# Kernel optimization log

Hardware: AMD Instinct MI355X
Metric: run time of the kernel (lower is better)

Reference implementation:

```python
import jax, jax.numpy as jnp
import numpy as np

B, N, C, H = 32, 577, 768, 12
D = C // H  # head_dim = 64


def _rotate_half(t):
    half = t.shape[-1] // 2
    return jnp.concatenate([-t[..., half:], t[..., :half]], axis=-1)


def _rope(t, sin, cos):
    # t: [B, H, N-1, D]; sin/cos: [N-1, D] broadcast over batch and heads
    return t * cos + _rotate_half(t) * sin


def setup_inputs() -> dict:
    key = jax.random.key(0)
    ks = jax.random.split(key, 5)
    x = jax.random.normal(ks[0], (B, N, C), dtype=jnp.float32)
    w_qkv = jax.random.normal(ks[1], (C, 3 * C), dtype=jnp.float32) * (1.0 / np.sqrt(C))
    b_qkv = jnp.zeros((3 * C,), dtype=jnp.float32)
    w_proj = jax.random.normal(ks[2], (C, C), dtype=jnp.float32) * (1.0 / np.sqrt(C))
    b_proj = jnp.zeros((C,), dtype=jnp.float32)
    # rotary tables for the N-1 non-CLS tokens
    pos = jnp.arange(N - 1, dtype=jnp.float32)[:, None]            # [N-1, 1]
    inv_freq = 1.0 / (10000.0 ** (jnp.arange(0, D, 2, dtype=jnp.float32) / D))  # [D/2]
    ang = pos * inv_freq[None, :]                                   # [N-1, D/2]
    ang = jnp.concatenate([ang, ang], axis=-1)                      # [N-1, D]
    rope_sin = jnp.sin(ang)
    rope_cos = jnp.cos(ang)
    return {"x": x, "w_qkv": w_qkv, "b_qkv": b_qkv, "w_proj": w_proj,
            "b_proj": b_proj, "rope_sin": rope_sin, "rope_cos": rope_cos}


def reference(x, w_qkv, b_qkv, w_proj, b_proj, rope_sin, rope_cos):
    Bx, Nx, Cx = x.shape
    qkv = x @ w_qkv + b_qkv                                   # [B, N, 3C]
    qkv = qkv.reshape(Bx, Nx, 3, H, D).transpose(2, 0, 3, 1, 4)  # [3, B, H, N, D]
    q, k, v = qkv[0], qkv[1], qkv[2]
    # RoPE only on non-CLS tokens (index 0 is CLS)
    q = jnp.concatenate([q[:, :, :1, :], _rope(q[:, :, 1:, :], rope_sin, rope_cos)], axis=2)
    k = jnp.concatenate([k[:, :, :1, :], _rope(k[:, :, 1:, :], rope_sin, rope_cos)], axis=2)
    q = q / jnp.sqrt(jnp.float32(D))
    attn = jnp.einsum("bhqd,bhkd->bhqk", q, k)               # [B, H, N, N]
    attn = jax.nn.softmax(attn.astype(jnp.float32), axis=-1).astype(x.dtype)
    out = jnp.einsum("bhqk,bhkd->bhqd", attn, v)             # [B, H, N, D]
    out = out.transpose(0, 2, 1, 3).reshape(Bx, Nx, Cx)       # [B, N, C]
    return out @ w_proj + b_proj
```

## Files before the change

kernel.cpp:

```cpp
#include <hip/hip_runtime.h>

#define Bdim 32
#define Ndim 577
#define Cdim 768
#define Hdim 12
#define Ddim 64
#define Mdim (Bdim*Ndim)
#define VSTRIDE 640

typedef __attribute__((ext_vector_type(4))) float f32x4;
typedef __attribute__((ext_vector_type(8))) __bf16 bf16x8;
typedef __attribute__((ext_vector_type(4))) __bf16 bf16x4;

__device__ __forceinline__ void gl_lds16(const __bf16* g, __bf16* l) {
  __builtin_amdgcn_global_load_lds((const __attribute__((address_space(1))) void*)g,
                                   (__attribute__((address_space(3))) void*)l, 16, 0, 0);
}

__global__ __launch_bounds__(256) void f32_to_bf16(const float4* __restrict__ in,
                                                   bf16x4* __restrict__ out, int n4) {
  int i = blockIdx.x * 256 + threadIdx.x;
  if (i < n4) {
    float4 v = in[i];
    bf16x4 o = {(__bf16)v.x, (__bf16)v.y, (__bf16)v.z, (__bf16)v.w};
    out[i] = o;
  }
}

__global__ __launch_bounds__(256) void transpose_f32_bf16(const float* __restrict__ in,
                                                          __bf16* __restrict__ out,
                                                          int R, int Cc) {
  __shared__ float tile[64][65];
  int bx = blockIdx.x * 64;
  int by = blockIdx.y * 64;
  int tx = threadIdx.x & 63, ty = threadIdx.x >> 6;
  for (int i = ty; i < 64; i += 4) {
    int r = by + i, c = bx + tx;
    tile[i][tx] = (r < R && c < Cc) ? in[(size_t)r * Cc + c] : 0.f;
  }
  __syncthreads();
  for (int i = ty; i < 64; i += 4) {
    int r = bx + i, c = by + tx;
    if (r < Cc && c < R) out[(size_t)r * R + c] = (__bf16)tile[tx][i];
  }
}

__device__ __forceinline__ void gemm_bt_core(const __bf16* __restrict__ A,
                                             const __bf16* __restrict__ BT,
                                             int m0, int n0,
                                             __bf16* As, __bf16* Bs,
                                             f32x4 acc[4][4]) {
  const int t = threadIdx.x;
  const int lane = t & 63, w = t >> 6;
  const int quad = lane >> 4, l16 = lane & 15;
  const int wm = w >> 1, wn = w & 1;
  const int srow = t >> 2, scol = (t & 3) * 8;

  for (int k0 = 0; k0 < 768; k0 += 32) {
    __syncthreads();
    #pragma unroll
    for (int p = 0; p < 2; ++p) {
      int row = p * 64 + srow;
      int ar = m0 + row; if (ar > Mdim - 1) ar = Mdim - 1;
      gl_lds16(A  + (size_t)ar * 768 + k0 + scol,        As + row * 32 + scol);
      gl_lds16(BT + (size_t)(n0 + row) * 768 + k0 + scol, Bs + row * 32 + scol);
    }
    __syncthreads();
    bf16x8 a[4], b[4];
    #pragma unroll
    for (int i = 0; i < 4; ++i) {
      a[i] = *(const bf16x8*)(As + (wm * 64 + i * 16 + l16) * 32 + quad * 8);
      b[i] = *(const bf16x8*)(Bs + (wn * 64 + i * 16 + l16) * 32 + quad * 8);
    }
    #pragma unroll
    for (int mt = 0; mt < 4; ++mt)
      #pragma unroll
      for (int nt = 0; nt < 4; ++nt)
        acc[mt][nt] = __builtin_amdgcn_mfma_f32_16x16x32_bf16(a[mt], b[nt], acc[mt][nt], 0, 0, 0);
  }
}

__global__ __launch_bounds__(256) void qkv_kernel(const __bf16* __restrict__ x,
                                                  const __bf16* __restrict__ wqkvT,
                                                  const float* __restrict__ b_qkv,
                                                  const float* __restrict__ rs,
                                                  const float* __restrict__ rc,
                                                  __bf16* __restrict__ q,
                                                  __bf16* __restrict__ k,
                                                  __bf16* __restrict__ vt) {
  __shared__ __bf16 As[128 * 32];
  __shared__ __bf16 Bs[128 * 32];
  f32x4 acc[4][4];
  const f32x4 fz = {0.f, 0.f, 0.f, 0.f};
  for (int i = 0; i < 4; ++i) for (int j = 0; j < 4; ++j) acc[i][j] = fz;

  const int m0 = blockIdx.x * 128, n0 = blockIdx.y * 128;
  gemm_bt_core(x, wqkvT, m0, n0, As, Bs, acc);

  const int lane = threadIdx.x & 63, w = threadIdx.x >> 6;
  const int quad = lane >> 4, l16 = lane & 15;
  const int wm = w >> 1, wn = w & 1;
  const int colbase = n0 + wn * 64;
  const int matrix = colbase / 768;
  const int head = (colbase % 768) / 64;

  #pragma unroll
  for (int mt = 0; mt < 4; ++mt) {
    int mbase = m0 + wm * 64 + mt * 16 + quad * 4;
    #pragma unroll
    for (int r = 0; r < 4; ++r) {
      int m = mbase + r;
      if (m >= Mdim) continue;
      int bb = m / 577, tok = m % 577;
      #pragma unroll
      for (int nt = 0; nt < 4; ++nt) {
        int d = nt * 16 + l16;
        float val = acc[mt][nt][r] + b_qkv[colbase + d];
        if (matrix == 2) {
          vt[((size_t)(bb * 12 + head) * 64 + d) * VSTRIDE + tok] = (__bf16)val;
        } else {
          if (tok > 0) {
            float partner = acc[mt][nt ^ 2][r] + b_qkv[colbase + (d ^ 32)];
            float sn = rs[(size_t)(tok - 1) * 64 + d];
            float cs = rc[(size_t)(tok - 1) * 64 + d];
            float rot = (d < 32) ? -partner : partner;
            val = val * cs + rot * sn;
          }
          __bf16* dst;
          if (matrix == 0) { val *= 0.125f; dst = q; } else dst = k;
          dst[((size_t)(bb * 12 + head) * 577 + tok) * 64 + d] = (__bf16)val;
        }
      }
    }
  }
}

__global__ __launch_bounds__(256) void attn_kernel(const __bf16* __restrict__ q,
                                                   const __bf16* __restrict__ k,
                                                   const __bf16* __restrict__ vt,
                                                   __bf16* __restrict__ ao) {
  __shared__ __bf16 qs[4096];
  __shared__ __bf16 ks[4096];
  __shared__ __bf16 vs[4096];
  __shared__ __bf16 ps[64 * 72];

  const int bh = blockIdx.x / 10;
  const int qt = blockIdx.x % 10;
  const int t = threadIdx.x;
  const int lane = t & 63, w = t >> 6;
  const int quad = lane >> 4, l16 = lane & 15;

  const __bf16* qbase = q + (size_t)bh * 577 * 64;
  const __bf16* kbase = k + (size_t)bh * 577 * 64;
  const __bf16* vbase = vt + (size_t)bh * 64 * VSTRIDE;

  #pragma unroll
  for (int p = 0; p < 2; ++p) {
    int g = p * 256 + t;
    int d8 = g >> 6, tok = g & 63;
    gl_lds16(qbase + (size_t)(qt * 64 + tok) * 64 + d8 * 8, qs + (size_t)g * 8);
  }

  f32x4 O[4]; const f32x4 fz = {0.f, 0.f, 0.f, 0.f};
  for (int i = 0; i < 4; ++i) O[i] = fz;
  float m_i[4], l_i[4];
  for (int r = 0; r < 4; ++r) { m_i[r] = -1e30f; l_i[r] = 0.f; }

  for (int kt = 0; kt < 10; ++kt) {
    __syncthreads();
    #pragma unroll
    for (int p = 0; p < 2; ++p) {
      int g = p * 256 + t;
      int d8 = g >> 6, tok = g & 63;
      gl_lds16(kbase + (size_t)(kt * 64 + tok) * 64 + d8 * 8, ks + (size_t)g * 8);
      gl_lds16(vbase + (size_t)(g & 63) * VSTRIDE + kt * 64 + (g >> 6) * 8, vs + (size_t)g * 8);
    }
    __syncthreads();

    f32x4 S[4]; for (int i = 0; i < 4; ++i) S[i] = fz;
    #pragma unroll
    for (int step = 0; step < 2; ++step) {
      bf16x8 a = *(const bf16x8*)(qs + (size_t)((step * 4 + quad) * 64 + w * 16 + l16) * 8);
      #pragma unroll
      for (int nt = 0; nt < 4; ++nt) {
        bf16x8 b = *(const bf16x8*)(ks + (size_t)((step * 4 + quad) * 64 + nt * 16 + l16) * 8);
        S[nt] = __builtin_amdgcn_mfma_f32_16x16x32_bf16(a, b, S[nt], 0, 0, 0);
      }
    }

    int kv_left = 577 - kt * 64;
    if (kv_left < 64) {
      #pragma unroll
      for (int nt = 0; nt < 4; ++nt) {
        int c = nt * 16 + l16;
        if (c >= kv_left) { S[nt][0] = -1e30f; S[nt][1] = -1e30f; S[nt][2] = -1e30f; S[nt][3] = -1e30f; }
      }
    }

    #pragma unroll
    for (int r = 0; r < 4; ++r) {
      float v = fmaxf(fmaxf(S[0][r], S[1][r]), fmaxf(S[2][r], S[3][r]));
      v = fmaxf(v, __shfl_xor(v, 1)); v = fmaxf(v, __shfl_xor(v, 2));
      v = fmaxf(v, __shfl_xor(v, 4)); v = fmaxf(v, __shfl_xor(v, 8));
      float newm = fmaxf(m_i[r], v);
      float alpha = __expf(m_i[r] - newm);
      m_i[r] = newm;
      float rsum = 0.f;
      #pragma unroll
      for (int nt = 0; nt < 4; ++nt) {
        float e = __expf(S[nt][r] - newm);
        rsum += e;
        ps[(size_t)(w * 16 + quad * 4 + r) * 72 + nt * 16 + l16] = (__bf16)e;
      }
      rsum += __shfl_xor(rsum, 1); rsum += __shfl_xor(rsum, 2);
      rsum += __shfl_xor(rsum, 4); rsum += __shfl_xor(rsum, 8);
      l_i[r] = l_i[r] * alpha + rsum;
      #pragma unroll
      for (int dt = 0; dt < 4; ++dt) O[dt][r] *= alpha;
    }

    #pragma unroll
    for (int step = 0; step < 2; ++step) {
      bf16x8 a = *(const bf16x8*)(ps + (size_t)(w * 16 + l16) * 72 + step * 32 + quad * 8);
      #pragma unroll
      for (int dt = 0; dt < 4; ++dt) {
        bf16x8 b = *(const bf16x8*)(vs + (size_t)((step * 4 + quad) * 64 + dt * 16 + l16) * 8);
        O[dt] = __builtin_amdgcn_mfma_f32_16x16x32_bf16(a, b, O[dt], 0, 0, 0);
      }
    }
  }

  const int bb = bh / 12, hh = bh % 12;
  const int qrow0 = qt * 64 + w * 16 + quad * 4;
  #pragma unroll
  for (int r = 0; r < 4; ++r) {
    int row = qrow0 + r;
    if (row < 577) {
      float inv = 1.f / l_i[r];
      size_t base = ((size_t)(bb * 577 + row)) * 768 + hh * 64;
      #pragma unroll
      for (int dt = 0; dt < 4; ++dt)
        ao[base + dt * 16 + l16] = (__bf16)(O[dt][r] * inv);
    }
  }
}

__global__ __launch_bounds__(256) void proj_kernel(const __bf16* __restrict__ ao,
                                                   const __bf16* __restrict__ wprojT,
                                                   const float* __restrict__ b_proj,
                                                   float* __restrict__ out) {
  __shared__ __bf16 As[128 * 32];
  __shared__ __bf16 Bs[128 * 32];
  f32x4 acc[4][4];
  const f32x4 fz = {0.f, 0.f, 0.f, 0.f};
  for (int i = 0; i < 4; ++i) for (int j = 0; j < 4; ++j) acc[i][j] = fz;

  const int m0 = blockIdx.x * 128, n0 = blockIdx.y * 128;
  gemm_bt_core(ao, wprojT, m0, n0, As, Bs, acc);

  const int lane = threadIdx.x & 63, w = threadIdx.x >> 6;
  const int quad = lane >> 4, l16 = lane & 15;
  const int wm = w >> 1, wn = w & 1;
  const int colbase = n0 + wn * 64;

  #pragma unroll
  for (int mt = 0; mt < 4; ++mt) {
    int mbase = m0 + wm * 64 + mt * 16 + quad * 4;
    #pragma unroll
    for (int r = 0; r < 4; ++r) {
      int m = mbase + r;
      if (m >= Mdim) continue;
      #pragma unroll
      for (int nt = 0; nt < 4; ++nt) {
        int c = colbase + nt * 16 + l16;
        out[(size_t)m * 768 + c] = acc[mt][nt][r] + b_proj[c];
      }
    }
  }
}

extern "C" void kernel_launch(void* const* d_in, const int* in_sizes, int n_in,
                              void* d_out, int out_size, void* d_ws, size_t ws_size,
                              hipStream_t stream) {
  const float* x      = (const float*)d_in[0];
  const float* w_qkv  = (const float*)d_in[1];
  const float* b_qkv  = (const float*)d_in[2];
  const float* w_proj = (const float*)d_in[3];
  const float* b_proj = (const float*)d_in[4];
  const float* rsn    = (const float*)d_in[5];
  const float* rcs    = (const float*)d_in[6];
  float* out = (float*)d_out;

  constexpr size_t QK_E = (size_t)Bdim * Hdim * Ndim * Ddim;
  constexpr size_t VT_E = (size_t)Bdim * Hdim * Ddim * VSTRIDE;
  constexpr size_t AO_E = (size_t)Mdim * Cdim;
  __bf16* q      = (__bf16*)d_ws;
  __bf16* k      = q + QK_E;
  __bf16* vt     = k + QK_E;
  __bf16* ao     = vt + VT_E;
  __bf16* xb     = ao;
  __bf16* wqkvT  = ao + AO_E;
  __bf16* wprojT = wqkvT + (size_t)2304 * 768;

  f32_to_bf16<<<13848, 256, 0, stream>>>((const float4*)x, (bf16x4*)xb,
                                         (int)(AO_E / 4));
  transpose_f32_bf16<<<dim3(36, 12), 256, 0, stream>>>(w_qkv, wqkvT, 768, 2304);
  transpose_f32_bf16<<<dim3(12, 12), 256, 0, stream>>>(w_proj, wprojT, 768, 768);
  qkv_kernel<<<dim3(145, 18), 256, 0, stream>>>(xb, wqkvT, b_qkv, rsn, rcs, q, k, vt);
  attn_kernel<<<3840, 256, 0, stream>>>(q, k, vt, ao);
  proj_kernel<<<dim3(145, 6), 256, 0, stream>>>(ao, wprojT, b_proj, out);
}
```

Before: 512.1 us.

## Stage V transpose through LDS and swap GEMM grid order for A-tile reuse

The QKV kernel's V epilogue now writes each 128-token by 64-dim tile into a padded shared-memory buffer and reads it back transposed. Stores to the transposed V buffer then cover consecutive tokens per dim row instead of scattering across rows with a 1280-byte stride. Both GEMM kernels also swap grid axes so blocks sharing an M row-tile launch together, which should improve L2 reuse of the activation tile. The cost is extra LDS, two barriers per half, and per-element index arithmetic; the global writes are still 2-byte scalar stores.

```diff
diff --git a/kernel.cpp b/kernel.cpp
--- a/kernel.cpp
+++ b/kernel.cpp
@@ -7,6 +7,7 @@
 #define Ddim 64
 #define Mdim (Bdim*Ndim)
 #define VSTRIDE 640
+#define TSTRIDE 152
 
 typedef __attribute__((ext_vector_type(4))) float f32x4;
 typedef __attribute__((ext_vector_type(8))) __bf16 bf16x8;
@@ -90,35 +91,72 @@
                                                   __bf16* __restrict__ vt) {
   __shared__ __bf16 As[128 * 32];
   __shared__ __bf16 Bs[128 * 32];
+  __shared__ __bf16 Ts[64 * TSTRIDE];
   f32x4 acc[4][4];
   const f32x4 fz = {0.f, 0.f, 0.f, 0.f};
   for (int i = 0; i < 4; ++i) for (int j = 0; j < 4; ++j) acc[i][j] = fz;
 
-  const int m0 = blockIdx.x * 128, n0 = blockIdx.y * 128;
+  const int n0 = blockIdx.x * 128;
+  const int m0 = blockIdx.y * 128;
   gemm_bt_core(x, wqkvT, m0, n0, As, Bs, acc);
 
-  const int lane = threadIdx.x & 63, w = threadIdx.x >> 6;
+  const int t = threadIdx.x;
+  const int lane = t & 63, w = t >> 6;
   const int quad = lane >> 4, l16 = lane & 15;
   const int wm = w >> 1, wn = w & 1;
   const int colbase = n0 + wn * 64;
   const int matrix = colbase / 768;
   const int head = (colbase % 768) / 64;
 
-  #pragma unroll
-  for (int mt = 0; mt < 4; ++mt) {
-    int mbase = m0 + wm * 64 + mt * 16 + quad * 4;
-    #pragma unroll
-    for (int r = 0; r < 4; ++r) {
-      int m = mbase + r;
-      if (m >= Mdim) continue;
-      int bb = m / 577, tok = m % 577;
-      #pragma unroll
-      for (int nt = 0; nt < 4; ++nt) {
-        int d = nt * 16 + l16;
-        float val = acc[mt][nt][r] + b_qkv[colbase + d];
-        if (matrix == 2) {
-          vt[((size_t)(bb * 12 + head) * 64 + d) * VSTRIDE + tok] = (__bf16)val;
-        } else {
+  if (matrix == 2) {
+    #pragma unroll
+    for (int h = 0; h < 2; ++h) {
+      __syncthreads();
+      if (wn == h) {
+        #pragma unroll
+        for (int mt = 0; mt < 4; ++mt) {
+          int tokbase = wm * 64 + mt * 16 + quad * 4;
+          #pragma unroll
+          for (int r = 0; r < 4; ++r) {
+            #pragma unroll
+            for (int nt = 0; nt < 4; ++nt) {
+              int dl = nt * 16 + l16;
+              Ts[dl * TSTRIDE + tokbase + r] =
+                  (__bf16)(acc[mt][nt][r] + b_qkv[colbase + dl]);
+            }
+          }
+        }
+      }
+      __syncthreads();
+      int hh = (n0 + h * 64 - 1536) / 64;
+      #pragma unroll
+      for (int it = 0; it < 4; ++it) {
+        int c = it * 256 + t;
+        int dl = c >> 4, chunk = c & 15;
+        bf16x8 vv = *(const bf16x8*)(Ts + dl * TSTRIDE + chunk * 8);
+        #pragma unroll
+        for (int j = 0; j < 8; ++j) {
+          int m = m0 + chunk * 8 + j;
+          if (m < Mdim) {
+            int bb = m / 577, tok = m % 577;
+            vt[((size_t)(bb * 12 + hh) * 64 + dl) * VSTRIDE + tok] = vv[j];
+          }
+        }
+      }
+    }
+  } else {
+    #pragma unroll
+    for (int mt = 0; mt < 4; ++mt) {
+      int mbase = m0 + wm * 64 + mt * 16 + quad * 4;
+      #pragma unroll
+      for (int r = 0; r < 4; ++r) {
+        int m = mbase + r;
+        if (m >= Mdim) continue;
+        int bb = m / 577, tok = m % 577;
+        #pragma unroll
+        for (int nt = 0; nt < 4; ++nt) {
+          int d = nt * 16 + l16;
+          float val = acc[mt][nt][r] + b_qkv[colbase + d];
           if (tok > 0) {
             float partner = acc[mt][nt ^ 2][r] + b_qkv[colbase + (d ^ 32)];
             float sn = rs[(size_t)(tok - 1) * 64 + d];
@@ -255,7 +293,8 @@
   const f32x4 fz = {0.f, 0.f, 0.f, 0.f};
   for (int i = 0; i < 4; ++i) for (int j = 0; j < 4; ++j) acc[i][j] = fz;
 
-  const int m0 = blockIdx.x * 128, n0 = blockIdx.y * 128;
+  const int n0 = blockIdx.x * 128;
+  const int m0 = blockIdx.y * 128;
   gemm_bt_core(ao, wprojT, m0, n0, As, Bs, acc);
 
   const int lane = threadIdx.x & 63, w = threadIdx.x >> 6;
@@ -306,7 +345,7 @@
                                          (int)(AO_E / 4));
   transpose_f32_bf16<<<dim3(36, 12), 256, 0, stream>>>(w_qkv, wqkvT, 768, 2304);
   transpose_f32_bf16<<<dim3(12, 12), 256, 0, stream>>>(w_proj, wprojT, 768, 768);
-  qkv_kernel<<<dim3(145, 18), 256, 0, stream>>>(xb, wqkvT, b_qkv, rsn, rcs, q, k, vt);
+  qkv_kernel<<<dim3(18, 145), 256, 0, stream>>>(xb, wqkvT, b_qkv, rsn, rcs, q, k, vt);
   attn_kernel<<<3840, 256, 0, stream>>>(q, k, vt, ao);
-  proj_kernel<<<dim3(145, 6), 256, 0, stream>>>(ao, wprojT, b_proj, out);
-}
+  proj_kernel<<<dim3(6, 145), 256, 0, stream>>>(ao, wprojT, b_proj, out);
+}
```

Measured after the change: 516.9 us. About the same (+0.9%).
